# Optimization experiments

Hardware: AMD Instinct MI355X
Metric: run time of the kernel (lower is better)

The kernel has to match this reference:

```python
import jax, jax.numpy as jnp
import numpy as np

N = 8192
E_DIM = 256
HID = 256
OUT = 128
N_PRED = 2_000_000


def setup_inputs() -> dict:
    key = jax.random.key(0)
    ks = jax.random.split(key, 6)
    node_indices = jnp.arange(N, dtype=jnp.int64) if jax.config.jax_enable_x64 else jnp.arange(N, dtype=jnp.int32)
    attn_matrix = jax.random.normal(ks[0], (N, N), dtype=jnp.float32)
    edge_label_index = jax.random.randint(ks[1], (2, N_PRED), 0, N)
    emb = jax.random.normal(ks[2], (N, E_DIM), dtype=jnp.float32) * 0.05
    W1 = jax.random.normal(ks[3], (E_DIM, HID), dtype=jnp.float32) * (1.0 / np.sqrt(E_DIM))
    b1 = jnp.zeros((HID,), dtype=jnp.float32)
    W2 = jax.random.normal(ks[4], (HID, OUT), dtype=jnp.float32) * (1.0 / np.sqrt(HID))
    b2 = jnp.zeros((OUT,), dtype=jnp.float32)
    return {"node_indices": node_indices, "attn_matrix": attn_matrix,
            "edge_label_index": edge_label_index, "emb": emb,
            "W1": W1, "b1": b1, "W2": W2, "b2": b2}


def reference(node_indices, attn_matrix, edge_label_index, emb, W1, b1, W2, b2):
    # dense_to_sparse of an (almost surely) all-nonzero dense matrix keeps all
    # N^2 edges (incl. diagonal), so no extra self-loops are added by gcn_norm.
    w = jax.nn.relu(attn_matrix)                       # edge weights after F.relu
    deg = w.sum(axis=0)                                # deg[j] = sum_i w[i,j] (scatter on col)
    dis = jnp.where(deg > 0, jax.lax.rsqrt(deg), 0.0)  # deg^{-1/2}, inf -> 0
    a_norm = dis[:, None] * w * dis[None, :]           # norm_ij = d_i^-1/2 w_ij d_j^-1/2

    x = emb[node_indices]                              # embedding lookup [N, E_DIM]
    # GCNConv: aggregate transformed features at target (col): out = A_norm^T @ (x W) + b
    h = jax.nn.relu(a_norm.T @ (x @ W1) + b1)          # [N, HID]
    z = a_norm.T @ (h @ W2) + b2                       # [N, OUT]

    # decode: dot product between endpoint embeddings
    scores = jnp.einsum('ed,ed->e', z[edge_label_index[0]], z[edge_label_index[1]])
    return scores
```

## Files before the change

### kernel.cpp

```cpp
#include <hip/hip_runtime.h>

typedef _Float16 half8  __attribute__((ext_vector_type(8)));
typedef _Float16 half4v __attribute__((ext_vector_type(4)));
typedef _Float16 half2v __attribute__((ext_vector_type(2)));
typedef float    floatx4 __attribute__((ext_vector_type(4)));
typedef float    f4v     __attribute__((ext_vector_type(4)));

#define NND 8192
#define PA  40
#define PT  136

__device__ __forceinline__ int swzk(int m, int k) { return k ^ (((m >> 3) & 3) << 3); }

#define GLOAD16(gp, lp) __builtin_amdgcn_global_load_lds(                        \
    (const __attribute__((address_space(1))) void*)(gp),                         \
    (__attribute__((address_space(3))) void*)(lp), 16, 0, 0)

__global__ __launch_bounds__(256) void k_degT(const float* __restrict__ A,
                                              _Float16* __restrict__ Wh,
                                              float* __restrict__ deg) {
    __shared__ _Float16 T[128 * PT];
    __shared__ float sdeg[8 * 128];
    int t  = threadIdx.x;
    int j0 = blockIdx.x * 128, i0 = blockIdx.y * 128;
    int c = t & 31;
    int g = t >> 5;

    f4v s = {0.f, 0.f, 0.f, 0.f};
    #pragma unroll
    for (int p = 0; p < 2; ++p) {
        int rb = 64 * p + 8 * g;
        f4v v[8];
        #pragma unroll
        for (int rr = 0; rr < 8; ++rr)
            v[rr] = *(const f4v*)(A + (size_t)(i0 + rb + rr) * NND + j0 + 4 * c);
        #pragma unroll
        for (int rr = 0; rr < 8; ++rr)
            #pragma unroll
            for (int u = 0; u < 4; ++u) v[rr][u] = fmaxf(v[rr][u], 0.f);
        #pragma unroll
        for (int u = 0; u < 4; ++u) {
            half8 hv;
            #pragma unroll
            for (int rr = 0; rr < 8; ++rr) { hv[rr] = (_Float16)v[rr][u]; s[u] += v[rr][u]; }
            *(half8*)(&T[(4 * c + u) * PT + rb]) = hv;
        }
    }
    *(f4v*)(&sdeg[g * 128 + 4 * c]) = s;
    __syncthreads();

    if (t < 128) {
        float d = 0.f;
        #pragma unroll
        for (int g2 = 0; g2 < 8; ++g2) d += sdeg[g2 * 128 + t];
        atomicAdd(&deg[j0 + t], d);
    }

    #pragma unroll
    for (int p = 0; p < 8; ++p) {
        int j  = 16 * p + (t >> 4);
        int ic = (t & 15) * 8;
        half8 hv = *(const half8*)(&T[j * PT + ic]);
        *(half8*)(Wh + (size_t)(j0 + j) * NND + i0 + ic) = hv;
    }
}

__global__ __launch_bounds__(256) void k_dis(const float* __restrict__ deg, float* __restrict__ dis) {
    int j = blockIdx.x * 256 + threadIdx.x;
    float d = deg[j];
    dis[j] = d > 0.f ? 1.f / sqrtf(d) : 0.f;
}

template <typename AT>
__global__ __launch_bounds__(256) void k_mm_small(
    const AT* __restrict__ Abase, const int* __restrict__ gather,
    const float* __restrict__ B, int NB,
    _Float16* __restrict__ outT, const float* __restrict__ dis, float out_scale) {

    __shared__ _Float16 As[128 * PA];
    __shared__ _Float16 Bs[64 * PA];

    int t  = threadIdx.x;
    int i0 = blockIdx.x * 128;
    int n0 = blockIdx.y * 64;

    int am = t & 127, akh = t >> 7;
    int row = i0 + am;
    if (gather) row = gather[row];
    const AT* arow = Abase + (size_t)row * 256;

    int tp = t & 15, kp = t >> 4;

    int lane = t & 63, w = t >> 6;
    int wm = w & 1, wn = w >> 1;
    int lm = lane & 15, q = lane >> 4;

    floatx4 acc[4][2];
    #pragma unroll
    for (int a = 0; a < 4; ++a)
        #pragma unroll
        for (int b = 0; b < 2; ++b) acc[a][b] = (floatx4){0.f, 0.f, 0.f, 0.f};

    for (int ks = 0; ks < 8; ++ks) {
        int c0 = ks * 32;

        half8 av[2];
        if constexpr (sizeof(AT) == 4) {
            #pragma unroll
            for (int cc = 0; cc < 2; ++cc) {
                f4v v0 = *(const f4v*)(arow + c0 + akh * 16 + cc * 8);
                f4v v1 = *(const f4v*)(arow + c0 + akh * 16 + cc * 8 + 4);
                half8 hv;
                #pragma unroll
                for (int e = 0; e < 4; ++e) {
                    hv[e]     = (_Float16)(16.f * v0[e]);
                    hv[4 + e] = (_Float16)(16.f * v1[e]);
                }
                av[cc] = hv;
            }
        } else {
            av[0] = *(const half8*)(arow + c0 + akh * 16);
            av[1] = *(const half8*)(arow + c0 + akh * 16 + 8);
        }

        const float* bp = B + (size_t)(c0 + 2 * kp) * NB + n0 + 4 * tp;
        f4v r0 = *(const f4v*)bp;
        f4v r1 = *(const f4v*)(bp + NB);

        __syncthreads();
        #pragma unroll
        for (int cc = 0; cc < 2; ++cc) {
            int k = akh * 16 + cc * 8;
            *(half8*)(&As[am * PA + swzk(am, k)]) = av[cc];
        }
        #pragma unroll
        for (int u = 0; u < 4; ++u) {
            int n = 4 * tp + u;
            half2v p = {(_Float16)r0[u], (_Float16)r1[u]};
            *(half2v*)(&Bs[n * PA + swzk(n, 2 * kp)]) = p;
        }
        __syncthreads();

        half8 af[4], bf[2];
        #pragma unroll
        for (int mt = 0; mt < 4; ++mt) {
            int m = wm * 64 + mt * 16 + lm;
            af[mt] = *(const half8*)(&As[m * PA + swzk(m, q * 8)]);
        }
        #pragma unroll
        for (int nt = 0; nt < 2; ++nt) {
            int n = wn * 32 + nt * 16 + lm;
            bf[nt] = *(const half8*)(&Bs[n * PA + swzk(n, q * 8)]);
        }
        #pragma unroll
        for (int mt = 0; mt < 4; ++mt)
            #pragma unroll
            for (int nt = 0; nt < 2; ++nt)
                acc[mt][nt] = __builtin_amdgcn_mfma_f32_16x16x32_f16(af[mt], bf[nt], acc[mt][nt], 0, 0, 0);
    }

    #pragma unroll
    for (int mt = 0; mt < 4; ++mt) {
        int ib = i0 + wm * 64 + mt * 16 + q * 4;
        #pragma unroll
        for (int nt = 0; nt < 2; ++nt) {
            int n = n0 + wn * 32 + nt * 16 + lm;
            #pragma unroll
            for (int r = 0; r < 4; ++r) {
                float v = acc[mt][nt][r] * dis[ib + r] * out_scale;
                outT[(size_t)n * NND + ib + r] = (_Float16)v;
            }
        }
    }
}

template <int BN>
__global__ __launch_bounds__(256) void k_mm_big(
    const _Float16* __restrict__ Wh, const _Float16* __restrict__ Bt, float* __restrict__ Cp) {

    __shared__ __align__(16) _Float16 As[128 * 32];
    __shared__ __align__(16) _Float16 Bs[128 * 32];

    int t = threadIdx.x;
    int j0 = blockIdx.x * 128;
    int n0 = blockIdx.y * 128;
    size_t i_begin = (size_t)blockIdx.z * 1024;
    float* C = Cp + (size_t)blockIdx.z * (size_t)NND * BN;

    int lane = t & 63, w = t >> 6;
    int wm = w & 1, wn = w >> 1;
    int lm = lane & 15, q = lane >> 4;

    int srow = lane >> 2;
    int scol = (lane & 3) * 8;
    const _Float16* aS0 = Wh + (size_t)(j0 + w * 16 + srow) * NND + i_begin + scol;
    const _Float16* aS1 = aS0 + (size_t)64 * NND;
    const _Float16* bS0 = Bt + (size_t)(n0 + w * 16 + srow) * NND + i_begin + scol;
    const _Float16* bS1 = bS0 + (size_t)64 * NND;

    char* aL0 = (char*)As + w * 1024;
    char* aL1 = (char*)As + (4 + w) * 1024;
    char* bL0 = (char*)Bs + w * 1024;
    char* bL1 = (char*)Bs + (4 + w) * 1024;

    floatx4 acc[4][4];
    #pragma unroll
    for (int a = 0; a < 4; ++a)
        #pragma unroll
        for (int b = 0; b < 4; ++b) acc[a][b] = (floatx4){0.f, 0.f, 0.f, 0.f};

    for (int ks = 0; ks < 32; ++ks) {
        int ko = ks * 32;
        GLOAD16(aS0 + ko, aL0);
        GLOAD16(aS1 + ko, aL1);
        GLOAD16(bS0 + ko, bL0);
        GLOAD16(bS1 + ko, bL1);
        __syncthreads();

        half8 af[4], bf[4];
        #pragma unroll
        for (int mt = 0; mt < 4; ++mt) {
            int m = wm * 64 + mt * 16 + lm;
            af[mt] = *(const half8*)(&As[m * 32 + q * 8]);
        }
        #pragma unroll
        for (int nt = 0; nt < 4; ++nt) {
            int n = wn * 64 + nt * 16 + lm;
            bf[nt] = *(const half8*)(&Bs[n * 32 + q * 8]);
        }
        #pragma unroll
        for (int mt = 0; mt < 4; ++mt)
            #pragma unroll
            for (int nt = 0; nt < 4; ++nt)
                acc[mt][nt] = __builtin_amdgcn_mfma_f32_16x16x32_f16(af[mt], bf[nt], acc[mt][nt], 0, 0, 0);
        __syncthreads();
    }

    #pragma unroll
    for (int mt = 0; mt < 4; ++mt) {
        int rb = j0 + wm * 64 + mt * 16 + q * 4;
        #pragma unroll
        for (int nt = 0; nt < 4; ++nt) {
            int col = n0 + wn * 64 + nt * 16 + lm;
            #pragma unroll
            for (int r = 0; r < 4; ++r)
                C[(size_t)(rb + r) * BN + col] = acc[mt][nt][r];
        }
    }
}

template <int NSH, bool RELU>
__global__ __launch_bounds__(256) void k_finalize(const float* __restrict__ Cp, const float* __restrict__ dis,
                                                  const float* __restrict__ bias, _Float16* __restrict__ out) {
    int idx = blockIdx.x * 256 + threadIdx.x;
    float v = 0.f;
    #pragma unroll
    for (int z = 0; z < 8; ++z) v += Cp[(size_t)z * (NND << NSH) + idx];
    int j = idx >> NSH;
    int n = idx & ((1 << NSH) - 1);
    v = v * (1.f / 1024.f) * dis[j] + bias[n];
    if (RELU) v = fmaxf(v, 0.f);
    out[idx] = (_Float16)(v * 64.f);
}

__global__ __launch_bounds__(256) void k_edges(const _Float16* __restrict__ zh, const int* __restrict__ ei,
                                               float* __restrict__ out, int npred) {
    int g = (blockIdx.x * 256 + threadIdx.x) >> 4;
    int l = threadIdx.x & 15;
    if (g >= npred) return;
    int a = ei[g], b = ei[npred + g];
    half8 za = *(const half8*)(zh + (size_t)a * 128 + l * 8);
    half8 zb = *(const half8*)(zh + (size_t)b * 128 + l * 8);
    float s = 0.f;
    #pragma unroll
    for (int e = 0; e < 8; ++e) s += (float)za[e] * (float)zb[e];
    s += __shfl_xor(s, 1);
    s += __shfl_xor(s, 2);
    s += __shfl_xor(s, 4);
    s += __shfl_xor(s, 8);
    if (l == 0) out[g] = s * (1.f / 4096.f);
}

extern "C" void kernel_launch(void* const* d_in, const int* in_sizes, int n_in,
                              void* d_out, int out_size, void* d_ws, size_t ws_size,
                              hipStream_t stream) {
    const int*   nodes = (const int*)d_in[0];
    const float* attn  = (const float*)d_in[1];
    const int*   eidx  = (const int*)d_in[2];
    const float* emb   = (const float*)d_in[3];
    const float* W1    = (const float*)d_in[4];
    const float* b1    = (const float*)d_in[5];
    const float* W2    = (const float*)d_in[6];
    const float* b2    = (const float*)d_in[7];
    float* out = (float*)d_out;
    int npred = in_sizes[2] / 2;

    char* ws = (char*)d_ws;
    float*    deg = (float*)(ws);
    float*    dis = (float*)(ws + 0x8000);
    _Float16* Wh  = (_Float16*)(ws + 0x10000);
    float*    C1p = (float*)(ws + 0x8010000);
    float*    C2p = (float*)(ws + 0xC010000);
    _Float16* M1p = (_Float16*)(ws + 0xE010000);
    _Float16* h   = (_Float16*)(ws + 0xE410000);
    _Float16* M2p = (_Float16*)(ws + 0xE810000);
    _Float16* zh  = (_Float16*)(ws + 0xEA10000);

    hipMemsetAsync(deg, 0, 8192 * sizeof(float), stream);

    k_degT<<<dim3(64, 64), 256, 0, stream>>>(attn, Wh, deg);
    k_dis<<<32, 256, 0, stream>>>(deg, dis);

    k_mm_small<float><<<dim3(64, 4), 256, 0, stream>>>(emb, nodes, W1, 256, M1p, dis, 64.f);
    k_mm_big<256><<<dim3(64, 2, 8), 256, 0, stream>>>(Wh, M1p, C1p);
    k_finalize<8, true><<<8192, 256, 0, stream>>>(C1p, dis, b1, h);
    k_mm_small<_Float16><<<dim3(64, 2), 256, 0, stream>>>(h, nullptr, W2, 128, M2p, dis, 16.f);
    k_mm_big<128><<<dim3(64, 1, 8), 256, 0, stream>>>(Wh, M2p, C2p);
    k_finalize<7, false><<<4096, 256, 0, stream>>>(C2p, dis, b2, zh);

    k_edges<<<(npred + 15) / 16, 256, 0, stream>>>(zh, eidx, out, npred);
}
```

Measured before the change: 642.3 us.

## Double-buffer big GEMM LDS loads, vectorize finalize, use fdot2 in edge scoring

Result: no change. 641.1 us (-0.2%).

```diff
diff --git a/kernel.cpp b/kernel.cpp
--- a/kernel.cpp
+++ b/kernel.cpp
@@ -15,6 +15,8 @@
 #define GLOAD16(gp, lp) __builtin_amdgcn_global_load_lds(                        \
     (const __attribute__((address_space(1))) void*)(gp),                         \
     (__attribute__((address_space(3))) void*)(lp), 16, 0, 0)
+
+#define VMCNT0() asm volatile("s_waitcnt vmcnt(0)" ::: "memory")
 
 __global__ __launch_bounds__(256) void k_degT(const float* __restrict__ A,
                                               _Float16* __restrict__ Wh,
@@ -178,8 +180,8 @@
 __global__ __launch_bounds__(256) void k_mm_big(
     const _Float16* __restrict__ Wh, const _Float16* __restrict__ Bt, float* __restrict__ Cp) {
 
-    __shared__ __align__(16) _Float16 As[128 * 32];
-    __shared__ __align__(16) _Float16 Bs[128 * 32];
+    __shared__ __align__(16) _Float16 As[2 * 128 * 32];
+    __shared__ __align__(16) _Float16 Bs[2 * 128 * 32];
 
     int t = threadIdx.x;
     int j0 = blockIdx.x * 128;
@@ -198,10 +200,8 @@
     const _Float16* bS0 = Bt + (size_t)(n0 + w * 16 + srow) * NND + i_begin + scol;
     const _Float16* bS1 = bS0 + (size_t)64 * NND;
 
-    char* aL0 = (char*)As + w * 1024;
-    char* aL1 = (char*)As + (4 + w) * 1024;
-    char* bL0 = (char*)Bs + w * 1024;
-    char* bL1 = (char*)Bs + (4 + w) * 1024;
+    char* aLb = (char*)As + w * 1024;
+    char* bLb = (char*)Bs + w * 1024;
 
     floatx4 acc[4][4];
     #pragma unroll
@@ -209,31 +209,49 @@
         #pragma unroll
         for (int b = 0; b < 4; ++b) acc[a][b] = (floatx4){0.f, 0.f, 0.f, 0.f};
 
+    {
+        GLOAD16(aS0, aLb);
+        GLOAD16(aS1, aLb + 4096);
+        GLOAD16(bS0, bLb);
+        GLOAD16(bS1, bLb + 4096);
+    }
+    VMCNT0();
+    __builtin_amdgcn_s_barrier();
+
     for (int ks = 0; ks < 32; ++ks) {
-        int ko = ks * 32;
-        GLOAD16(aS0 + ko, aL0);
-        GLOAD16(aS1 + ko, aL1);
-        GLOAD16(bS0 + ko, bL0);
-        GLOAD16(bS1 + ko, bL1);
-        __syncthreads();
+        int cur = ks & 1;
+        const _Float16* Ab = As + cur * 4096;
+        const _Float16* Bb = Bs + cur * 4096;
+
+        if (ks < 31) {
+            int ko = (ks + 1) * 32;
+            char* aL = aLb + (cur ^ 1) * 8192;
+            char* bL = bLb + (cur ^ 1) * 8192;
+            GLOAD16(aS0 + ko, aL);
+            GLOAD16(aS1 + ko, aL + 4096);
+            GLOAD16(bS0 + ko, bL);
+            GLOAD16(bS1 + ko, bL + 4096);
+        }
 
         half8 af[4], bf[4];
         #pragma unroll
         for (int mt = 0; mt < 4; ++mt) {
             int m = wm * 64 + mt * 16 + lm;
-            af[mt] = *(const half8*)(&As[m * 32 + q * 8]);
+            af[mt] = *(const half8*)(&Ab[m * 32 + q * 8]);
         }
         #pragma unroll
         for (int nt = 0; nt < 4; ++nt) {
             int n = wn * 64 + nt * 16 + lm;
-            bf[nt] = *(const half8*)(&Bs[n * 32 + q * 8]);
+            bf[nt] = *(const half8*)(&Bb[n * 32 + q * 8]);
         }
         #pragma unroll
         for (int mt = 0; mt < 4; ++mt)
             #pragma unroll
             for (int nt = 0; nt < 4; ++nt)
                 acc[mt][nt] = __builtin_amdgcn_mfma_f32_16x16x32_f16(af[mt], bf[nt], acc[mt][nt], 0, 0, 0);
-        __syncthreads();
+
+        VMCNT0();
+        __builtin_amdgcn_s_barrier();
     }
 
     #pragma unroll
@@ -252,15 +270,26 @@
 template <int NSH, bool RELU>
 __global__ __launch_bounds__(256) void k_finalize(const float* __restrict__ Cp, const float* __restrict__ dis,
                                                   const float* __restrict__ bias, _Float16* __restrict__ out) {
-    int idx = blockIdx.x * 256 + threadIdx.x;
-    float v = 0.f;
-    #pragma unroll
-    for (int z = 0; z < 8; ++z) v += Cp[(size_t)z * (NND << NSH) + idx];
-    int j = idx >> NSH;
-    int n = idx & ((1 << NSH) - 1);
-    v = v * (1.f / 1024.f) * dis[j] + bias[n];
-    if (RELU) v = fmaxf(v, 0.f);
-    out[idx] = (_Float16)(v * 64.f);
+    int idx4 = (blockIdx.x * 256 + threadIdx.x) * 4;
+    f4v v = {0.f, 0.f, 0.f, 0.f};
+    #pragma unroll
+    for (int z = 0; z < 8; ++z) {
+        f4v p = *(const f4v*)(Cp + (size_t)z * (NND << NSH) + idx4);
+        #pragma unroll
+        for (int r = 0; r < 4; ++r) v[r] += p[r];
+    }
+    int j  = idx4 >> NSH;
+    int n0 = idx4 & ((1 << NSH) - 1);
+    float dj = dis[j] * (1.f / 1024.f);
+    f4v b4 = *(const f4v*)(bias + n0);
+    half4v o;
+    #pragma unroll
+    for (int r = 0; r < 4; ++r) {
+        float x = v[r] * dj + b4[r];
+        if (RELU) x = fmaxf(x, 0.f);
+        o[r] = (_Float16)(x * 64.f);
+    }
+    *(half4v*)(out + idx4) = o;
 }
 
 __global__ __launch_bounds__(256) void k_edges(const _Float16* __restrict__ zh, const int* __restrict__ ei,
@@ -273,7 +302,11 @@
     half8 zb = *(const half8*)(zh + (size_t)b * 128 + l * 8);
     float s = 0.f;
     #pragma unroll
-    for (int e = 0; e < 8; ++e) s += (float)za[e] * (float)zb[e];
+    for (int e = 0; e < 4; ++e) {
+        half2v a2 = {za[2 * e], za[2 * e + 1]};
+        half2v b2 = {zb[2 * e], zb[2 * e + 1]};
+        s = __builtin_amdgcn_fdot2(a2, b2, s, false);
+    }
     s += __shfl_xor(s, 1);
     s += __shfl_xor(s, 2);
     s += __shfl_xor(s, 4);
@@ -313,10 +346,10 @@
 
     k_mm_small<float><<<dim3(64, 4), 256, 0, stream>>>(emb, nodes, W1, 256, M1p, dis, 64.f);
     k_mm_big<256><<<dim3(64, 2, 8), 256, 0, stream>>>(Wh, M1p, C1p);
-    k_finalize<8, true><<<8192, 256, 0, stream>>>(C1p, dis, b1, h);
+    k_finalize<8, true><<<2048, 256, 0, stream>>>(C1p, dis, b1, h);
     k_mm_small<_Float16><<<dim3(64, 2), 256, 0, stream>>>(h, nullptr, W2, 128, M2p, dis, 16.f);
     k_mm_big<128><<<dim3(64, 1, 8), 256, 0, stream>>>(Wh, M2p, C2p);
-    k_finalize<7, false><<<4096, 256, 0, stream>>>(C2p, dis, b2, zh);
+    k_finalize<7, false><<<1024, 256, 0, stream>>>(C2p, dis, b2, zh);
 
     k_edges<<<(npred + 15) / 16, 256, 0, stream>>>(zh, eidx, out, npred);
 }
```
